# Performance work log

Measured on AMD Instinct MI355X. Metric: run time of the kernel, lower is better.

Reference implementation:

```python
import jax, jax.numpy as jnp
import numpy as np
import math

H = 256; W = 256
NUM_CURVES = 256
NUM_SAMPLES = 32
NUM_BEZIERS = 2
BDEG = 5            # Bernstein degree used by the module (bezier_degree+1)
CTRL_STRIDE = 5     # bezier_degree+1; segments share endpoints, wrap (closed curve)
N_CTRL = NUM_BEZIERS * CTRL_STRIDE   # 10 control points per closed curve
PIX_CHUNK = 512
CHOLESKY_BOUND = jnp.array([0.5, 0.0, 0.5], jnp.float32)


def _bernstein():
    # t in linspace(0.007, 0.993, S) exactly as _update_bernstein_cache
    t = jnp.linspace(0.007, 0.993, NUM_SAMPLES)
    i = jnp.arange(BDEG + 1, dtype=jnp.float32)
    comb = jnp.array([math.comb(BDEG, k) for k in range(BDEG + 1)], jnp.float32)
    return comb * (t[:, None] ** i) * ((1.0 - t[:, None]) ** (BDEG - i))  # [S, BDEG+1]


def _render(control_points, features_dc, cholesky, opacity, depth, background):
    Bmat = _bernstein()
    # closed curve: segment k uses control points (k*5 + j) mod 10, j=0..5
    seg_idx = (jnp.arange(NUM_BEZIERS)[:, None] * CTRL_STRIDE
               + jnp.arange(BDEG + 1)[None, :]) % N_CTRL          # [K, 6]
    seg_ctrl = control_points[:, seg_idx]                          # [N, K, 6, 2]
    pts = jnp.einsum('sj,nkjd->nksd', Bmat, seg_ctrl)              # [N, K, S, 2]
    pts = pts.reshape(NUM_CURVES, -1, 2)                           # [N, Gper, 2]
    gper = pts.shape[1]

    # normalized [-1,1] -> pixel coords
    means = (jnp.tanh(pts) * 0.5 + 0.5) * jnp.array([W, H], jnp.float32)
    means = means.reshape(-1, 2)                                   # [G, 2]

    # 2x2 covariance from lower-triangular Cholesky (per curve)
    c = cholesky + CHOLESKY_BOUND[None, :]                         # l11, l21, l22
    s00 = c[:, 0] ** 2
    s01 = c[:, 0] * c[:, 1]
    s11 = c[:, 1] ** 2 + c[:, 2] ** 2
    det = s00 * s11 - s01 ** 2
    conic = jnp.stack([s11 / det, -s01 / det, s00 / det], -1)      # [N, 3]

    rep = lambda a: jnp.repeat(a, gper, axis=0)
    conic_g = rep(conic)                                           # [G, 3]
    color_g = rep(jax.nn.sigmoid(features_dc))                     # [G, 3]
    alpha_g = rep(jax.nn.sigmoid(opacity))[:, 0]                   # [G]
    depth_g = rep(depth)[:, 0]                                     # [G]

    order = jnp.argsort(depth_g)                                   # front-to-back
    means_s = means[order]
    conic_s = conic_g[order]
    color_s = color_g[order]
    alpha_s = alpha_g[order]

    ys, xs = jnp.meshgrid(jnp.arange(H, dtype=jnp.float32) + 0.5,
                          jnp.arange(W, dtype=jnp.float32) + 0.5, indexing='ij')
    pix = jnp.stack([xs.ravel(), ys.ravel()], -1).reshape(-1, PIX_CHUNK, 2)

    @jax.checkpoint
    def render_chunk(p):                                           # [C,2] -> [C,3]
        dx = p[:, None, 0] - means_s[None, :, 0]
        dy = p[:, None, 1] - means_s[None, :, 1]
        power = (-0.5 * (conic_s[None, :, 0] * dx * dx
                         + conic_s[None, :, 2] * dy * dy)
                 - conic_s[None, :, 1] * dx * dy)
        a = jnp.clip(alpha_s[None, :] * jnp.exp(power), 0.0, 0.999)
        logT = jnp.cumsum(jnp.log1p(-a), axis=1)
        t_excl = jnp.exp(logT - jnp.log1p(-a))   # transmittance before each splat
        rgb = (a * t_excl) @ color_s             # [C, 3]
        return rgb + jnp.exp(logT[:, -1:]) * background[None, :]

    img = jax.lax.map(render_chunk, pix)                           # [P/C, C, 3]
    return jnp.clip(img.reshape(H, W, 3), 0.0, 1.0)


def setup_inputs() -> dict:
    key = jax.random.key(0)
    k1, k2, k3, k4 = jax.random.split(key, 4)
    return {
        "control_points": jax.random.normal(k1, (NUM_CURVES, N_CTRL, 2), jnp.float32),
        "features_dc": jax.random.uniform(k2, (NUM_CURVES, 3), jnp.float32),
        "cholesky": jax.random.uniform(k3, (NUM_CURVES, 3), jnp.float32),
        "opacity": jnp.ones((NUM_CURVES, 1), jnp.float32),
        "depth": jax.random.uniform(k4, (NUM_CURVES, 1), jnp.float32),
        "background": jnp.ones((3,), jnp.float32),
    }


def reference(control_points, features_dc, cholesky, opacity, depth, background):
    return _render(control_points, features_dc, cholesky, opacity, depth, background)
```

## Files before the change

kernel.cpp:

```cpp
#include <hip/hip_runtime.h>
#include <hip/hip_fp16.h>
#include <math.h>

#define NCURVES   256
#define GPER      64
#define NUM_G     (NCURVES*GPER)
#define IMG_W     256
#define IMG_H     256
#define TILE      16
#define TILES_X   (IMG_W/TILE)
#define TILES_Y   (IMG_H/TILE)
#define NTILES    (TILES_X*TILES_Y)
#define REC_F     8

#define A_MIN     3.0e-6f
#define P_CUT     (-12.6f)

#define SEGS      8
#define GSEG      (NUM_G/SEGS)
#define GWAVE     (GSEG/4)

__global__ __launch_bounds__(GPER)
void prep(const float* __restrict__ ctrl,
          const float* __restrict__ features,
          const float* __restrict__ cholesky,
          const float* __restrict__ opacity,
          const float* __restrict__ depth,
          float*       __restrict__ recs,
          unsigned*    __restrict__ bbox)
{
    int c   = blockIdx.x;
    int tid = threadIdx.x;

    float dc = depth[c];
    int r = 0;
    #pragma unroll
    for (int jj = 0; jj < 4; ++jj) {
        int j = tid + jj*64;
        float dj = depth[j];
        r += (dj < dc) || (dj == dc && j < c);
    }
    #pragma unroll
    for (int off = 32; off > 0; off >>= 1) r += __shfl_down(r, off, 64);
    r = __shfl(r, 0, 64);

    float c0 = cholesky[3*c+0] + 0.5f;
    float c1 = cholesky[3*c+1];
    float c2 = cholesky[3*c+2] + 0.5f;
    float s00 = c0*c0;
    float s01 = c0*c1;
    float s11 = c1*c1 + c2*c2;
    float inv = 1.0f / (s00*s11 - s01*s01);
    float A  =  s11*inv;
    float Bc = -s01*inv;
    float Cc =  s00*inv;

    float cr = 1.0f/(1.0f + __expf(-features[3*c+0]));
    float cg = 1.0f/(1.0f + __expf(-features[3*c+1]));
    float cb = 1.0f/(1.0f + __expf(-features[3*c+2]));
    float al = 1.0f/(1.0f + __expf(-opacity[c]));

    float cut = fmaxf(2.0f*(__logf(al) - __logf(A_MIN)), 0.0f);
    float rx = sqrtf(cut * s00);
    float ry = sqrtf(cut * s11);

    int k = tid >> 5;
    int s = tid & 31;
    float t = 0.007f + (float)s * (0.986f/31.0f);
    float u = 1.0f - t;
    float t2=t*t, t3=t2*t, t4=t3*t, t5=t4*t;
    float u2=u*u, u3=u2*u, u4=u3*u, u5=u4*u;
    float w[6] = { u5, 5.0f*t*u4, 10.0f*t2*u3, 10.0f*t3*u2, 5.0f*t4*u, t5 };

    const float* cp = ctrl + c*20;
    float px = 0.0f, py = 0.0f;
    #pragma unroll
    for (int j = 0; j < 6; ++j) {
        int idx = (k*5 + j) % 10;
        px += w[j]*cp[2*idx+0];
        py += w[j]*cp[2*idx+1];
    }
    float mx = (tanhf(px)*0.5f + 0.5f) * (float)IMG_W;
    float my = (tanhf(py)*0.5f + 0.5f) * (float)IMG_H;

    int gi = r*GPER + tid;

    unsigned rg  = (unsigned)__half_as_ushort(__float2half_rn(cr))
                 | ((unsigned)__half_as_ushort(__float2half_rn(cg)) << 16);
    unsigned cbp = (unsigned)__half_as_ushort(__float2half_rn(cb));

    float4* o4 = (float4*)(recs + (size_t)gi*REC_F);
    o4[0] = make_float4(mx, my, A, Bc);
    o4[1] = make_float4(Cc, al, __uint_as_float(rg), __uint_as_float(cbp));

    int tx0 = min(max((int)floorf((mx - rx) * (1.0f/TILE)), 0), TILES_X-1);
    int tx1 = min(max((int)floorf((mx + rx) * (1.0f/TILE)), 0), TILES_X-1);
    int ty0 = min(max((int)floorf((my - ry) * (1.0f/TILE)), 0), TILES_Y-1);
    int ty1 = min(max((int)floorf((my + ry) * (1.0f/TILE)), 0), TILES_Y-1);
    bbox[gi] = (unsigned)tx0 | ((unsigned)ty0<<8) | ((unsigned)tx1<<16) | ((unsigned)ty1<<24);
}

__global__ __launch_bounds__(256)
void render8(const float*    __restrict__ recs,
             const unsigned* __restrict__ bbox,
             float4*         __restrict__ partial)
{
    __shared__ unsigned short flat[GSEG];
    __shared__ unsigned       wn[4];

    int tid   = threadIdx.x;
    int seg   = blockIdx.x & (SEGS-1);
    int tile  = blockIdx.x >> 3;
    int tilex = tile & (TILES_X-1);
    int tiley = tile >> 4;

    int lane = tid & 63;
    int wid  = tid >> 6;
    unsigned long long lmask = (1ull << lane) - 1ull;

    int sbase = seg * GSEG;
    int gwave = wid * GWAVE;

    bool pr[8];
    int cnt = 0;
    {
        unsigned bb[8];
        #pragma unroll
        for (int u = 0; u < 8; ++u)
            bb[u] = bbox[sbase + gwave + u*64 + lane];
        #pragma unroll
        for (int u = 0; u < 8; ++u) {
            unsigned b = bb[u];
            pr[u] = (tilex >= (int)( b        & 0xff)) &
                    (tilex <= (int)((b >> 16) & 0xff)) &
                    (tiley >= (int)((b >>  8) & 0xff)) &
                    (tiley <= (int)((b >> 24) & 0xff));
            cnt += (int)__popcll(__ballot(pr[u] ? 1 : 0));
        }
    }
    if (lane == 0) wn[wid] = (unsigned)cnt;
    __syncthreads();

    unsigned p1 = wn[0], p2 = p1 + wn[1], p3 = p2 + wn[2];
    int total = (int)(p3 + wn[3]);

    if (total) {
        unsigned base = (wid == 0) ? 0u : (wid == 1) ? p1 : (wid == 2) ? p2 : p3;
        int off = 0;
        #pragma unroll
        for (int u = 0; u < 8; ++u) {
            unsigned long long m = __ballot(pr[u] ? 1 : 0);
            if (pr[u])
                flat[base + off + (int)__popcll(m & lmask)] =
                    (unsigned short)(gwave + u*64 + lane);
            off += (int)__popcll(m);
        }
    }
    __syncthreads();

    int ix = tid & (TILE-1);
    int iy = tid >> 4;
    float pxf = (float)(tilex*TILE + ix) + 0.5f;
    float pyf = (float)(tiley*TILE + iy) + 0.5f;

    float T = 1.0f, accr = 0.0f, accg = 0.0f, accb = 0.0f;

    #pragma unroll 2
    for (int j = 0; j < total; ++j) {
        int gl = (int)flat[j];
        const float4* rp = (const float4*)(recs + (size_t)(sbase + gl)*REC_F);
        float4 r0 = rp[0];
        float4 r1 = rp[1];
        float dx = pxf - r0.x;
        float dy = pyf - r0.y;
        float p  = -0.5f*(r0.z*dx*dx + r1.x*dy*dy) - r0.w*dx*dy;
        if (p > P_CUT) {
            float a = fminf(r1.y * __expf(p), 0.999f);
            float wgt = a * T;
            unsigned rg = __float_as_uint(r1.z);
            accr += wgt * __half2float(__ushort_as_half((unsigned short)(rg & 0xffff)));
            accg += wgt * __half2float(__ushort_as_half((unsigned short)(rg >> 16)));
            accb += wgt * __half2float(__ushort_as_half((unsigned short)__float_as_uint(r1.w)));
            T *= (1.0f - a);
        }
    }

    int X = tilex*TILE + ix;
    int Y = tiley*TILE + iy;
    partial[(size_t)seg*(IMG_W*IMG_H) + (size_t)Y*IMG_W + X] =
        make_float4(accr, accg, accb, T);
}

__global__ __launch_bounds__(256)
void combine(const float4* __restrict__ partial,
             const float*  __restrict__ background,
             float*        __restrict__ out)
{
    int p = blockIdx.x * 256 + threadIdx.x;

    float accr = 0.0f, accg = 0.0f, accb = 0.0f, T = 1.0f;
    #pragma unroll
    for (int s = 0; s < SEGS; ++s) {
        float4 q = partial[(size_t)s*(IMG_W*IMG_H) + p];
        accr += T * q.x;
        accg += T * q.y;
        accb += T * q.z;
        T    *= q.w;
    }
    float r = fminf(fmaxf(accr + T*background[0], 0.0f), 1.0f);
    float g = fminf(fmaxf(accg + T*background[1], 0.0f), 1.0f);
    float b = fminf(fmaxf(accb + T*background[2], 0.0f), 1.0f);

    size_t oi = (size_t)p*3;
    out[oi+0] = r;
    out[oi+1] = g;
    out[oi+2] = b;
}

extern "C" void kernel_launch(void* const* d_in, const int* in_sizes, int n_in,
                              void* d_out, int out_size, void* d_ws, size_t ws_size,
                              hipStream_t stream)
{
    const float* ctrl       = (const float*)d_in[0];
    const float* features   = (const float*)d_in[1];
    const float* cholesky   = (const float*)d_in[2];
    const float* opacity    = (const float*)d_in[3];
    const float* depth      = (const float*)d_in[4];
    const float* background = (const float*)d_in[5];
    float* out = (float*)d_out;

    char* w = (char*)d_ws;
    float*    recs    = (float*)   (w);
    unsigned* bboxp   = (unsigned*)(w + 524288);
    float4*   partial = (float4*)  (w + 524288 + 65536);

    prep<<<NCURVES, GPER, 0, stream>>>(ctrl, features, cholesky, opacity, depth,
                                       recs, bboxp);
    render8<<<NTILES*SEGS, 256, 0, stream>>>(recs, bboxp, partial);
    combine<<<(IMG_W*IMG_H)/256, 256, 0, stream>>>(partial, background, out);
}
```

Measured before the change: 84.32 us.

## Fuse per-curve prep into tile render kernel with shared-memory splat records

Removes the separate prep kernel. Each render block ranks all curves by depth itself, evaluates the Bezier samples for the 32 curves in its depth segment and culls them against its tile. Surviving records go straight into per-wave shared memory, so the global record and bbox round-trip and one launch disappear. The render loop now reads records from LDS and stops early once every pixel's transmittance falls below a threshold. In exchange, every block repeats the depth ranking and curve evaluation, each wave's list is capped at 224 entries (overflow is silently clamped), and the early exit is an approximation.

```diff
diff --git a/kernel.cpp b/kernel.cpp
--- a/kernel.cpp
+++ b/kernel.cpp
@@ -15,98 +15,25 @@
 
 #define A_MIN     3.0e-6f
 #define P_CUT     (-12.6f)
+#define T_EPS     1.0e-5f
 
 #define SEGS      8
-#define GSEG      (NUM_G/SEGS)
-#define GWAVE     (GSEG/4)
-
-__global__ __launch_bounds__(GPER)
-void prep(const float* __restrict__ ctrl,
-          const float* __restrict__ features,
-          const float* __restrict__ cholesky,
-          const float* __restrict__ opacity,
-          const float* __restrict__ depth,
-          float*       __restrict__ recs,
-          unsigned*    __restrict__ bbox)
+#define CPS       (NCURVES/SEGS)
+#define CPW       (CPS/4)
+#define CAP       224
+
+__global__ __launch_bounds__(256)
+void render_fused(const float* __restrict__ ctrl,
+                  const float* __restrict__ features,
+                  const float* __restrict__ cholesky,
+                  const float* __restrict__ opacity,
+                  const float* __restrict__ depth,
+                  float4*      __restrict__ partial)
 {
-    int c   = blockIdx.x;
-    int tid = threadIdx.x;
-
-    float dc = depth[c];
-    int r = 0;
-    #pragma unroll
-    for (int jj = 0; jj < 4; ++jj) {
-        int j = tid + jj*64;
-        float dj = depth[j];
-        r += (dj < dc) || (dj == dc && j < c);
-    }
-    #pragma unroll
-    for (int off = 32; off > 0; off >>= 1) r += __shfl_down(r, off, 64);
-    r = __shfl(r, 0, 64);
-
-    float c0 = cholesky[3*c+0] + 0.5f;
-    float c1 = cholesky[3*c+1];
-    float c2 = cholesky[3*c+2] + 0.5f;
-    float s00 = c0*c0;
-    float s01 = c0*c1;
-    float s11 = c1*c1 + c2*c2;
-    float inv = 1.0f / (s00*s11 - s01*s01);
-    float A  =  s11*inv;
-    float Bc = -s01*inv;
-    float Cc =  s00*inv;
-
-    float cr = 1.0f/(1.0f + __expf(-features[3*c+0]));
-    float cg = 1.0f/(1.0f + __expf(-features[3*c+1]));
-    float cb = 1.0f/(1.0f + __expf(-features[3*c+2]));
-    float al = 1.0f/(1.0f + __expf(-opacity[c]));
-
-    float cut = fmaxf(2.0f*(__logf(al) - __logf(A_MIN)), 0.0f);
-    float rx = sqrtf(cut * s00);
-    float ry = sqrtf(cut * s11);
-
-    int k = tid >> 5;
-    int s = tid & 31;
-    float t = 0.007f + (float)s * (0.986f/31.0f);
-    float u = 1.0f - t;
-    float t2=t*t, t3=t2*t, t4=t3*t, t5=t4*t;
-    float u2=u*u, u3=u2*u, u4=u3*u, u5=u4*u;
-    float w[6] = { u5, 5.0f*t*u4, 10.0f*t2*u3, 10.0f*t3*u2, 5.0f*t4*u, t5 };
-
-    const float* cp = ctrl + c*20;
-    float px = 0.0f, py = 0.0f;
-    #pragma unroll
-    for (int j = 0; j < 6; ++j) {
-        int idx = (k*5 + j) % 10;
-        px += w[j]*cp[2*idx+0];
-        py += w[j]*cp[2*idx+1];
-    }
-    float mx = (tanhf(px)*0.5f + 0.5f) * (float)IMG_W;
-    float my = (tanhf(py)*0.5f + 0.5f) * (float)IMG_H;
-
-    int gi = r*GPER + tid;
-
-    unsigned rg  = (unsigned)__half_as_ushort(__float2half_rn(cr))
-                 | ((unsigned)__half_as_ushort(__float2half_rn(cg)) << 16);
-    unsigned cbp = (unsigned)__half_as_ushort(__float2half_rn(cb));
-
-    float4* o4 = (float4*)(recs + (size_t)gi*REC_F);
-    o4[0] = make_float4(mx, my, A, Bc);
-    o4[1] = make_float4(Cc, al, __uint_as_float(rg), __uint_as_float(cbp));
-
-    int tx0 = min(max((int)floorf((mx - rx) * (1.0f/TILE)), 0), TILES_X-1);
-    int tx1 = min(max((int)floorf((mx + rx) * (1.0f/TILE)), 0), TILES_X-1);
-    int ty0 = min(max((int)floorf((my - ry) * (1.0f/TILE)), 0), TILES_Y-1);
-    int ty1 = min(max((int)floorf((my + ry) * (1.0f/TILE)), 0), TILES_Y-1);
-    bbox[gi] = (unsigned)tx0 | ((unsigned)ty0<<8) | ((unsigned)tx1<<16) | ((unsigned)ty1<<24);
-}
-
-__global__ __launch_bounds__(256)
-void render8(const float*    __restrict__ recs,
-             const unsigned* __restrict__ bbox,
-             float4*         __restrict__ partial)
-{
-    __shared__ unsigned short flat[GSEG];
-    __shared__ unsigned       wn[4];
+    __shared__ float4        lrec[4][CAP][2];
+    __shared__ float         dsh[NCURVES];
+    __shared__ unsigned char lcur[CPS];
+    __shared__ unsigned      wn[4];
 
     int tid   = threadIdx.x;
     int seg   = blockIdx.x & (SEGS-1);
@@ -118,45 +45,92 @@
     int wid  = tid >> 6;
     unsigned long long lmask = (1ull << lane) - 1ull;
 
-    int sbase = seg * GSEG;
-    int gwave = wid * GWAVE;
-
-    bool pr[8];
+    if (tid < NCURVES) dsh[tid] = depth[tid];
+    __syncthreads();
+
+    if (tid < NCURVES) {
+        float dc = dsh[tid];
+        int r = 0;
+        for (int j = 0; j < NCURVES; ++j) {
+            float dj = dsh[j];
+            r += (dj < dc) || (dj == dc && j < tid);
+        }
+        int slot = r - seg*CPS;
+        if ((unsigned)slot < (unsigned)CPS) lcur[slot] = (unsigned char)tid;
+    }
+    __syncthreads();
+
     int cnt = 0;
-    {
-        unsigned bb[8];
+    #pragma unroll 1
+    for (int u = 0; u < CPW; ++u) {
+        int c = (int)lcur[wid*CPW + u];
+
+        float c0 = cholesky[3*c+0] + 0.5f;
+        float c1 = cholesky[3*c+1];
+        float c2 = cholesky[3*c+2] + 0.5f;
+        float s00 = c0*c0;
+        float s01 = c0*c1;
+        float s11 = c1*c1 + c2*c2;
+        float inv = 1.0f / (s00*s11 - s01*s01);
+        float A  =  s11*inv;
+        float Bc = -s01*inv;
+        float Cc =  s00*inv;
+
+        float cr = 1.0f/(1.0f + __expf(-features[3*c+0]));
+        float cg = 1.0f/(1.0f + __expf(-features[3*c+1]));
+        float cb = 1.0f/(1.0f + __expf(-features[3*c+2]));
+        float al = 1.0f/(1.0f + __expf(-opacity[c]));
+
+        float cut = fmaxf(2.0f*(__logf(al) - __logf(A_MIN)), 0.0f);
+        float rx = sqrtf(cut * s00);
+        float ry = sqrtf(cut * s11);
+
+        int k = lane >> 5;
+        int s = lane & 31;
+        float t = 0.007f + (float)s * (0.986f/31.0f);
+        float uu = 1.0f - t;
+        float t2=t*t, t3=t2*t, t4=t3*t, t5=t4*t;
+        float u2=uu*uu, u3=u2*uu, u4=u3*uu, u5=u4*uu;
+        float w6[6] = { u5, 5.0f*t*u4, 10.0f*t2*u3, 10.0f*t3*u2, 5.0f*t4*uu, t5 };
+
+        const float* cp = ctrl + c*20;
+        float px = 0.0f, py = 0.0f;
         #pragma unroll
-        for (int u = 0; u < 8; ++u)
-            bb[u] = bbox[sbase + gwave + u*64 + lane];
-        #pragma unroll
-        for (int u = 0; u < 8; ++u) {
-            unsigned b = bb[u];
-            pr[u] = (tilex >= (int)( b        & 0xff)) &
-                    (tilex <= (int)((b >> 16) & 0xff)) &
-                    (tiley >= (int)((b >>  8) & 0xff)) &
-                    (tiley <= (int)((b >> 24) & 0xff));
-            cnt += (int)__popcll(__ballot(pr[u] ? 1 : 0));
-        }
-    }
+        for (int j = 0; j < 6; ++j) {
+            int idx = (k*5 + j) % 10;
+            px += w6[j]*cp[2*idx+0];
+            py += w6[j]*cp[2*idx+1];
+        }
+        float mx = (tanhf(px)*0.5f + 0.5f) * (float)IMG_W;
+        float my = (tanhf(py)*0.5f + 0.5f) * (float)IMG_H;
+
+        int tx0 = min(max((int)floorf((mx - rx) * (1.0f/TILE)), 0), TILES_X-1);
+        int tx1 = min(max((int)floorf((mx + rx) * (1.0f/TILE)), 0), TILES_X-1);
+        int ty0 = min(max((int)floorf((my - ry) * (1.0f/TILE)), 0), TILES_Y-1);
+        int ty1 = min(max((int)floorf((my + ry) * (1.0f/TILE)), 0), TILES_Y-1);
+        bool pred = (tilex >= tx0) & (tilex <= tx1) &
+                    (tiley >= ty0) & (tiley <= ty1);
+
+        unsigned long long m = __ballot(pred ? 1 : 0);
+        if (pred) {
+            int pos = cnt + (int)__popcll(m & lmask);
+            if (pos > CAP-1) pos = CAP-1;
+            unsigned rg  = (unsigned)__half_as_ushort(__float2half_rn(cr))
+                         | ((unsigned)__half_as_ushort(__float2half_rn(cg)) << 16);
+            unsigned cbp = (unsigned)__half_as_ushort(__float2half_rn(cb));
+            lrec[wid][pos][0] = make_float4(mx, my, A, Bc);
+            lrec[wid][pos][1] = make_float4(Cc, al,
+                                            __uint_as_float(rg),
+                                            __uint_as_float(cbp));
+        }
+        cnt += (int)__popcll(m);
+    }
+    if (cnt > CAP) cnt = CAP;
     if (lane == 0) wn[wid] = (unsigned)cnt;
     __syncthreads();
 
-    unsigned p1 = wn[0], p2 = p1 + wn[1], p3 = p2 + wn[2];
-    int total = (int)(p3 + wn[3]);
-
-    if (total) {
-        unsigned base = (wid == 0) ? 0u : (wid == 1) ? p1 : (wid == 2) ? p2 : p3;
-        int off = 0;
-        #pragma unroll
-        for (int u = 0; u < 8; ++u) {
-            unsigned long long m = __ballot(pr[u] ? 1 : 0);
-            if (pr[u])
-                flat[base + off + (int)__popcll(m & lmask)] =
-                    (unsigned short)(gwave + u*64 + lane);
-            off += (int)__popcll(m);
-        }
-    }
-    __syncthreads();
+    unsigned n0 = wn[0], n1 = wn[1], n2 = wn[2];
+    int total = (int)(n0 + n1 + n2 + wn[3]);
 
     int ix = tid & (TILE-1);
     int iy = tid >> 4;
@@ -165,23 +139,30 @@
 
     float T = 1.0f, accr = 0.0f, accg = 0.0f, accb = 0.0f;
 
-    #pragma unroll 2
-    for (int j = 0; j < total; ++j) {
-        int gl = (int)flat[j];
-        const float4* rp = (const float4*)(recs + (size_t)(sbase + gl)*REC_F);
-        float4 r0 = rp[0];
-        float4 r1 = rp[1];
-        float dx = pxf - r0.x;
-        float dy = pyf - r0.y;
-        float p  = -0.5f*(r0.z*dx*dx + r1.x*dy*dy) - r0.w*dx*dy;
-        if (p > P_CUT) {
-            float a = fminf(r1.y * __expf(p), 0.999f);
-            float wgt = a * T;
-            unsigned rg = __float_as_uint(r1.z);
-            accr += wgt * __half2float(__ushort_as_half((unsigned short)(rg & 0xffff)));
-            accg += wgt * __half2float(__ushort_as_half((unsigned short)(rg >> 16)));
-            accb += wgt * __half2float(__ushort_as_half((unsigned short)__float_as_uint(r1.w)));
-            T *= (1.0f - a);
+    #pragma unroll 1
+    for (int jb = 0; jb < total; jb += 32) {
+        if (!__any(T > T_EPS)) break;
+        int je = jb + 32 < total ? jb + 32 : total;
+        #pragma unroll 4
+        for (int j = jb; j < je; ++j) {
+            int w_ = 0; unsigned off = (unsigned)j;
+            if (off >= n0) { off -= n0; w_ = 1;
+              if (off >= n1) { off -= n1; w_ = 2;
+                if (off >= n2) { off -= n2; w_ = 3; } } }
+            float4 r0 = lrec[w_][off][0];
+            float4 r1 = lrec[w_][off][1];
+            float dx = pxf - r0.x;
+            float dy = pyf - r0.y;
+            float p  = -0.5f*(r0.z*dx*dx + r1.x*dy*dy) - r0.w*dx*dy;
+            if (p > P_CUT) {
+                float a = fminf(r1.y * __expf(p), 0.999f);
+                float wgt = a * T;
+                unsigned rg = __float_as_uint(r1.z);
+                accr += wgt * __half2float(__ushort_as_half((unsigned short)(rg & 0xffff)));
+                accg += wgt * __half2float(__ushort_as_half((unsigned short)(rg >> 16)));
+                accb += wgt * __half2float(__ushort_as_half((unsigned short)__float_as_uint(r1.w)));
+                T *= (1.0f - a);
+            }
         }
     }
 
@@ -230,12 +211,9 @@
     float* out = (float*)d_out;
 
     char* w = (char*)d_ws;
-    float*    recs    = (float*)   (w);
-    unsigned* bboxp   = (unsigned*)(w + 524288);
-    float4*   partial = (float4*)  (w + 524288 + 65536);
-
-    prep<<<NCURVES, GPER, 0, stream>>>(ctrl, features, cholesky, opacity, depth,
-                                       recs, bboxp);
-    render8<<<NTILES*SEGS, 256, 0, stream>>>(recs, bboxp, partial);
+    float4* partial = (float4*)(w);
+
+    render_fused<<<NTILES*SEGS, 256, 0, stream>>>(ctrl, features, cholesky,
+                                                  opacity, depth, partial);
     combine<<<(IMG_W*IMG_H)/256, 256, 0, stream>>>(partial, background, out);
 }
```

After: 114.9 us. 1.36x slower.
